# Kernel tuning notes

Hardware: AMD Instinct MI355X
Metric: run time of the kernel (lower is better)

The kernel has to match this reference:

```python
import jax, jax.numpy as jnp
import numpy as np

B, C, OUT, H, W, M1, M2, HID = 4, 64, 64, 256, 256, 32, 32, 64
COORD = C + 1  # MLP input: channels + 1 coordinate


def _lin(key, fan_in, fan_out):
    lim = 1.0 / np.sqrt(fan_in)
    kw, kb = jax.random.split(key)
    Wm = jax.random.uniform(kw, (fan_in, fan_out), minval=-lim, maxval=lim, dtype=jnp.float32)
    b = jax.random.uniform(kb, (fan_out,), minval=-lim, maxval=lim, dtype=jnp.float32)
    return Wm, b


def setup_inputs() -> dict:
    key = jax.random.key(0)
    ks = jax.random.split(key, 12)
    x = jax.random.normal(ks[0], (B, C, H, W), dtype=jnp.float32)
    # basis_w MLP: (C+1) -> HID -> HID -> 2*M2
    wW0, wb0 = _lin(ks[1], COORD, HID)
    wW1, wb1 = _lin(ks[2], HID, HID)
    wW2, wb2 = _lin(ks[3], HID, 2 * M2)
    # basis_h MLP: (C+1) -> HID -> HID -> 2*M1
    hW0, hb0 = _lin(ks[4], COORD, HID)
    hW1, hb1 = _lin(ks[5], HID, HID)
    hW2, hb2 = _lin(ks[6], HID, 2 * M1)
    std = (1.0 / (C + OUT)) ** 0.5
    Wf_re = std * jax.random.normal(ks[7], (C, OUT, M1, M2), dtype=jnp.float32)
    Wf_im = std * jax.random.normal(ks[8], (C, OUT, M1, M2), dtype=jnp.float32)
    mixer_w, mixer_b = _lin(ks[9], OUT, OUT)
    mixer_w = mixer_w.T  # (out, in) conv1x1 layout
    sc_w, sc_b = _lin(ks[10], C, OUT)
    sc_w = sc_w.T
    return {
        "x": x,
        "wW0": wW0, "wb0": wb0, "wW1": wW1, "wb1": wb1, "wW2": wW2, "wb2": wb2,
        "hW0": hW0, "hb0": hb0, "hW1": hW1, "hb1": hb1, "hW2": hW2, "hb2": hb2,
        "Wf_re": Wf_re, "Wf_im": Wf_im,
        "mixer_w": mixer_w, "mixer_b": mixer_b,
        "sc_w": sc_w, "sc_b": sc_b,
    }


def _gelu(v):
    return jax.nn.gelu(v, approximate=False)  # torch GELU is exact erf


def _cmlp(x, W0, b0, W1, b1, W2, b2, m):
    h = _gelu(x @ W0 + b0)
    h = _gelu(h @ W1 + b1)
    o = h @ W2 + b2
    return jax.lax.complex(o[..., :m], o[..., m:])


def reference(x, wW0, wb0, wW1, wb1, wW2, wb2,
              hW0, hb0, hW1, hb1, hW2, hb2,
              Wf_re, Wf_im, mixer_w, mixer_b, sc_w, sc_b):
    Bb, Cc, Hh, Ww = x.shape
    # --- W-direction basis: input is (values, w-coord) per pixel ---
    wc = jnp.linspace(-1.0, 1.0, Ww, dtype=jnp.float32)
    w_in = jnp.concatenate(
        [jnp.transpose(x, (0, 2, 3, 1)),
         jnp.broadcast_to(wc[None, None, :, None], (Bb, Hh, Ww, 1))], axis=-1)
    wb = _cmlp(w_in, wW0, wb0, wW1, wb1, wW2, wb2, M2)  # (B,H,W,m2) complex
    xc = x.astype(jnp.complex64)
    # separable transform along W: contract W against runtime basis
    tfw = jnp.einsum('bchw,bhwm->bchm', xc, wb)  # (B,C,H,m2)
    # --- H-direction basis: input is real part of W-transform + h-coord ---
    hcv = jnp.linspace(-1.0, 1.0, Hh, dtype=jnp.float32)
    h_in = jnp.concatenate(
        [jnp.transpose(tfw.real, (0, 3, 2, 1)),
         jnp.broadcast_to(hcv[None, None, :, None], (Bb, M2, Hh, 1))], axis=-1)
    hb = _cmlp(h_in, hW0, hb0, hW1, hb1, hW2, hb2, M1)  # (B,m2,H,m1) complex
    tfhw = jnp.einsum('bchm,bmhk->bckm', tfw, hb)  # (B,C,m1,m2)
    Wf = jax.lax.complex(Wf_re, Wf_im)  # (C_in, C_out, m1, m2)
    proc = jnp.einsum('bixy,oixy->boxy', tfhw, Wf)  # (B,out,m1,m2)
    # inverse transforms with conjugate-transposed bases
    rec = jnp.einsum('bokm,bmhk->bohm', proc, jnp.conj(hb))  # (B,out,H,m2)
    spatial = jnp.einsum('bohm,bhwm->bohw', rec, jnp.conj(wb)).real / (Hh * Ww)
    y = jnp.einsum('bchw,oc->bohw', spatial, mixer_w) + mixer_b[None, :, None, None]
    y = _gelu(y)
    y = y + jnp.einsum('bchw,oc->bohw', x, sc_w) + sc_b[None, :, None, None]
    return _gelu(y)
```

## Files before the change

kernel.cpp:

```cpp
#include <hip/hip_runtime.h>
#include <math.h>


typedef __attribute__((ext_vector_type(8))) short bf16x8;
typedef __attribute__((ext_vector_type(4))) float f32x4;

__device__ __forceinline__ float gelu_f(float v) {
    const float u = v * 0.70710678118654752440f;
    const float xa = fabsf(u);
    const float t = __builtin_amdgcn_rcpf(fmaf(0.3275911f, xa, 1.0f));
    float p = fmaf(1.061405429f, t, -1.453152027f);
    p = fmaf(p, t, 1.421413741f);
    p = fmaf(p, t, -0.284496736f);
    p = fmaf(p, t, 0.254829592f);
    p *= t;
    const float e = __expf(-xa * xa);
    float erfv = fmaf(-p, e, 1.0f);
    erfv = (u < 0.0f) ? -erfv : erfv;
    return 0.5f * v * (1.0f + erfv);
}

__device__ __forceinline__ unsigned short f2b(float f) {
    union { float f; unsigned int u; } v; v.f = f;
    unsigned int u = v.u + 0x7FFFu + ((v.u >> 16) & 1u);
    return (unsigned short)(u >> 16);
}
__device__ __forceinline__ float b2f(unsigned short b) {
    union { unsigned int u; float f; } v; v.u = ((unsigned int)b) << 16;
    return v.f;
}

__device__ __forceinline__ ushort4 butterfly_xT(const float4 v, int q) {
    const float bx = __shfl_xor(v.x, 1);
    const float by = __shfl_xor(v.y, 1);
    const float bz = __shfl_xor(v.z, 1);
    const float bw = __shfl_xor(v.w, 1);
    float4 s1;
    s1.x = ((q & 1) == 0) ? v.x : by;
    s1.y = ((q & 1) == 0) ? bx  : v.y;
    s1.z = ((q & 1) == 0) ? v.z : bw;
    s1.w = ((q & 1) == 0) ? bz  : v.w;
    const float cx = __shfl_xor(s1.x, 2);
    const float cy = __shfl_xor(s1.y, 2);
    const float cz = __shfl_xor(s1.z, 2);
    const float cw = __shfl_xor(s1.w, 2);
    float4 s2;
    s2.x = ((q & 2) == 0) ? s1.x : cz;
    s2.y = ((q & 2) == 0) ? s1.y : cw;
    s2.z = ((q & 2) == 0) ? cx   : s1.z;
    s2.w = ((q & 2) == 0) ? cy   : s1.w;
    ushort4 u;
    u.x = f2b(s2.x); u.y = f2b(s2.y); u.z = f2b(s2.z); u.w = f2b(s2.w);
    return u;
}

__global__ void k_prep(const float* __restrict__ wW0, const float* __restrict__ wW1,
                       const float* __restrict__ wW2,
                       const float* __restrict__ hW0, const float* __restrict__ hW1,
                       const float* __restrict__ hW2,
                       unsigned short* __restrict__ wT0, unsigned short* __restrict__ wT1,
                       unsigned short* __restrict__ wT2,
                       unsigned short* __restrict__ hT0, unsigned short* __restrict__ hT1,
                       unsigned short* __restrict__ hT2)
{
    const int t = threadIdx.x;
    for (int idx = t; idx < 64 * 96; idx += 256) {
        const int o = idx / 96, k = idx % 96;
        wT0[idx] = (k < 65) ? f2b(wW0[k * 64 + o]) : (unsigned short)0;
        hT0[idx] = (k < 65) ? f2b(hW0[k * 64 + o]) : (unsigned short)0;
    }
    for (int idx = t; idx < 4096; idx += 256) {
        const int o = idx >> 6, k = idx & 63;
        wT1[idx] = f2b(wW1[k * 64 + o]);
        wT2[idx] = f2b(wW2[k * 64 + o]);
        hT1[idx] = f2b(hW1[k * 64 + o]);
        hT2[idx] = f2b(hW2[k * 64 + o]);
    }
}

__global__ __launch_bounds__(256) void k_psum(const float* __restrict__ src,
                                              float* __restrict__ dst,
                                              int nparts, int part_stride)
{
    const int i = (blockIdx.x * 256 + threadIdx.x) * 4;
    float4 acc = *(const float4*)&src[i];
    for (int p = 1; p < nparts; ++p) {
        const float4 v = *(const float4*)&src[(size_t)p * part_stride + i];
        acc.x += v.x; acc.y += v.y; acc.z += v.z; acc.w += v.w;
    }
    *(float4*)&dst[i] = acc;
}

__global__ __launch_bounds__(256) void k_psum_procT(const float* __restrict__ src,
                                                    float* __restrict__ dst)
{
    const int idx = blockIdx.x * 256 + threadIdx.x;
    const int o = idx & 63, k = (idx >> 6) & 31, m = (idx >> 11) & 31, b = idx >> 16;
    const size_t in = (size_t)(b * 64 + o) * 1024 + k * 32 + m;
    const float re = src[in] + src[524288 + in];
    const float im = src[262144 + in] + src[524288 + 262144 + in];
    dst[idx] = re;
    dst[262144 + idx] = im;
}

template<bool GELU, int NKC>
__device__ __forceinline__ void mfma_layer_r(
    const bf16x8* __restrict__ wf,
    const unsigned short* __restrict__ sAct,
    unsigned short* __restrict__ dst,
    const float4 bv, int arow, int g, int wv)
{
    const int crow = 16 * wv + g * 4;
    const int sx7 = arow & 7, sx3 = arow & 3;
    const f32x4 zero = {0.f, 0.f, 0.f, 0.f};
    f32x4 acc[4] = {zero, zero, zero, zero};
#pragma unroll
    for (int kc = 0; kc < NKC; ++kc) {
        const int chraw = kc * 4 + g;
        const int ch = (chraw < 8) ? (chraw ^ sx7) : (8 + ((chraw - 8) ^ sx3));
#pragma unroll
        for (int nt = 0; nt < 4; ++nt) {
            const bf16x8 b = *(const bf16x8*)&sAct[(nt * 16 + arow) * 96 + ch * 8];
            acc[nt] = __builtin_amdgcn_mfma_f32_16x16x32_bf16(wf[kc], b, acc[nt], 0, 0, 0);
        }
    }
    const int chw = (crow >> 3) ^ sx7;
#pragma unroll
    for (int nt = 0; nt < 4; ++nt) {
        const int px = nt * 16 + arow;
        float v0 = acc[nt][0] + bv.x;
        float v1 = acc[nt][1] + bv.y;
        float v2 = acc[nt][2] + bv.z;
        float v3 = acc[nt][3] + bv.w;
        if (GELU) { v0 = gelu_f(v0); v1 = gelu_f(v1); v2 = gelu_f(v2); v3 = gelu_f(v3); }
        ushort4 u;
        u.x = f2b(v0); u.y = f2b(v1); u.z = f2b(v2); u.w = f2b(v3);
        *(ushort4*)&dst[px * 96 + chw * 8 + (crow & 7)] = u;
    }
}

__global__ __launch_bounds__(256) void k_wbtfw(
    const float* __restrict__ x,
    const unsigned short* __restrict__ wT0, const float* __restrict__ b0,
    const unsigned short* __restrict__ wT1, const float* __restrict__ b1,
    const unsigned short* __restrict__ wT2, const float* __restrict__ b2,
    unsigned short* __restrict__ wb_bf, unsigned short* __restrict__ xT_bf,
    float* __restrict__ tfwM)
{
    __shared__ __align__(16) unsigned short smem[20480];
    unsigned short* sA   = smem;
    unsigned short* sB   = smem + 6144;
    unsigned short* sXt  = smem + 12288;
    unsigned short* sWBt = smem + 16384;

    const int bh = blockIdx.x;
    const int b = bh >> 8, h = bh & 255;
    const int t = threadIdx.x;
    const int lane = t & 63, wv = t >> 6;
    const int arow = lane & 15, g = lane >> 4;
    const int crow = 16 * wv + g * 4;
    const int sx7 = arow & 7;
    const f32x4 zero = {0.f, 0.f, 0.f, 0.f};

    const int wrow = 16 * wv + arow;
    bf16x8 w0f[3], w1f[2], w2f[2];
#pragma unroll
    for (int kc = 0; kc < 3; ++kc)
        w0f[kc] = *(const bf16x8*)&wT0[wrow * 96 + (kc * 4 + g) * 8];
#pragma unroll
    for (int kc = 0; kc < 2; ++kc) {
        w1f[kc] = *(const bf16x8*)&wT1[wrow * 64 + (kc * 4 + g) * 8];
        w2f[kc] = *(const bf16x8*)&wT2[wrow * 64 + (kc * 4 + g) * 8];
    }
    const float4 bv0 = *(const float4*)&b0[crow];
    const float4 bv1 = *(const float4*)&b1[crow];
    const float4 bv2 = *(const float4*)&b2[crow];

    f32x4 atf[4] = {zero, zero, zero, zero};

    for (int wq = 0; wq < 4; ++wq) {
        const int w0 = wq * 64;
        __syncthreads();
        {
            const int q = lane & 3, wg = lane >> 2;
#pragma unroll
            for (int r = 0; r < 4; ++r) {
                const int cb = 16 * r + 4 * wv;
                const int c = cb + q;
                const float4 v = *(const float4*)&x[((size_t)(b * 64 + c) * 256 + h) * 256 + w0 + wg * 4];
                ushort4 ux;
                ux.x = f2b(v.x); ux.y = f2b(v.y); ux.z = f2b(v.z); ux.w = f2b(v.w);
                const int chx = (wg >> 1) ^ (c & 7);
                *(ushort4*)&sXt[c * 64 + chx * 8 + 4 * (wg & 1)] = ux;
                const ushort4 u = butterfly_xT(v, q);
                const int row = wg * 4 + q;
                const int cha = (cb >> 3) ^ (row & 7);
                *(ushort4*)&sA[row * 96 + cha * 8 + (cb & 7)] = u;
            }
        }
        if (t < 64) {
            const uint4 z = {0, 0, 0, 0};
#pragma unroll
            for (int j = 0; j < 4; ++j)
                *(uint4*)&sA[t * 96 + (8 + (j ^ (t & 3))) * 8] = z;
            sA[t * 96 + (8 + (t & 3)) * 8] = f2b((float)(w0 + t) * (2.0f / 255.0f) - 1.0f);
        }
        __syncthreads();
        const size_t pixbase = (size_t)(b * 256 + h) * 256 + w0;
#pragma unroll
        for (int r = 0; r < 2; ++r) {
            const int idx = r * 256 + t;
            const int px = idx >> 3, f = idx & 7;
            *(uint4*)&xT_bf[(pixbase + px) * 64 + f * 8] =
                *(const uint4*)&sA[px * 96 + ((f ^ (px & 7)) << 3)];
        }
        mfma_layer_r<true, 3>(w0f, sA, sB, bv0, arow, g, wv);
        __syncthreads();
        mfma_layer_r<true, 2>(w1f, sB, sA, bv1, arow, g, wv);
        __syncthreads();
        {
            f32x4 acc[4] = {zero, zero, zero, zero};
#pragma unroll
            for (int kc = 0; kc < 2; ++kc) {
                const int ch = (kc * 4 + g) ^ sx7;
#pragma unroll
                for (int nt = 0; nt < 4; ++nt) {
                    const bf16x8 bb = *(const bf16x8*)&sA[(nt * 16 + arow) * 96 + ch * 8];
                    acc[nt] = __builtin_amdgcn_mfma_f32_16x16x32_bf16(w2f[kc], bb, acc[nt], 0, 0, 0);
                }
            }
            const int chw = (crow >> 3) ^ sx7;
#pragma unroll
            for (int nt = 0; nt < 4; ++nt) {
                const int px = nt * 16 + arow;
                ushort4 u;
                u.x = f2b(acc[nt][0] + bv2.x);
                u.y = f2b(acc[nt][1] + bv2.y);
                u.z = f2b(acc[nt][2] + bv2.z);
                u.w = f2b(acc[nt][3] + bv2.w);
                *(ushort4*)&sB[px * 96 + chw * 8 + (crow & 7)] = u;
                const int ph = px >> 3, pl = px & 7;
                sWBt[(crow + 0) * 64 + ((ph ^ ((crow + 0) & 7)) << 3) + pl] = u.x;
                sWBt[(crow + 1) * 64 + ((ph ^ ((crow + 1) & 7)) << 3) + pl] = u.y;
                sWBt[(crow + 2) * 64 + ((ph ^ ((crow + 2) & 7)) << 3) + pl] = u.z;
                sWBt[(crow + 3) * 64 + ((ph ^ ((crow + 3) & 7)) << 3) + pl] = u.w;
            }
        }
        __syncthreads();
#pragma unroll
        for (int r = 0; r < 2; ++r) {
            const int idx = r * 256 + t;
            const int px = idx >> 3, f = idx & 7;
            *(uint4*)&wb_bf[(pixbase + px) * 64 + f * 8] =
                *(const uint4*)&sB[px * 96 + ((f ^ (px & 7)) << 3)];
        }
#pragma unroll
        for (int kc = 0; kc < 2; ++kc) {
            const int ch = (kc * 4 + g) ^ sx7;
            const bf16x8 a = *(const bf16x8*)&sWBt[(16 * wv + arow) * 64 + ch * 8];
#pragma unroll
            for (int nt = 0; nt < 4; ++nt) {
                const bf16x8 bb = *(const bf16x8*)&sXt[(nt * 16 + arow) * 64 + ch * 8];
                atf[nt] = __builtin_amdgcn_mfma_f32_16x16x32_bf16(a, bb, atf[nt], 0, 0, 0);
            }
        }
    }

    __syncthreads();
    float* sF = (float*)smem;
#pragma unroll
    for (int nt = 0; nt < 4; ++nt) {
        const int c = nt * 16 + arow;
#pragma unroll
        for (int j = 0; j < 4; ++j)
            sF[(crow + j) * 68 + c] = atf[nt][j];
    }
    __syncthreads();
#pragma unroll
    for (int r = 0; r < 4; ++r) {
        const int idx = r * 256 + t;
        const int m = idx >> 5, gg = idx & 31;
        float4 v;
        v.x = sF[m * 68 + gg * 2];
        v.y = sF[(m + 32) * 68 + gg * 2];
        v.z = sF[m * 68 + gg * 2 + 1];
        v.w = sF[(m + 32) * 68 + gg * 2 + 1];
        *(float4*)&tfwM[((size_t)(b * 32 + m) * 256 + h) * 128 + gg * 4] = v;
    }
}

__global__ __launch_bounds__(256) void k_hb_mlp3(
    const float* __restrict__ tfwM,
    const unsigned short* __restrict__ hT0, const float* __restrict__ b0,
    const unsigned short* __restrict__ hT1, const float* __restrict__ b1,
    const unsigned short* __restrict__ hT2, const float* __restrict__ b2,
    unsigned short* __restrict__ hb_bf)
{
    __shared__ __align__(16) unsigned short sA[64 * 96];
    __shared__ __align__(16) unsigned short sB[64 * 96];
    const int blk = blockIdx.x;
    const int bm = blk >> 2, hq = blk & 3;
    const int h0 = hq * 64;
    const int t = threadIdx.x;
    const int lane = t & 63, wv = t >> 6;
    const int arow = lane & 15, g = lane >> 4;
    const int crow = 16 * wv + g * 4;

    const int wrow = 16 * wv + arow;
    bf16x8 h0f[3], h1f[2], h2f[2];
#pragma unroll
    for (int kc = 0; kc < 3; ++kc)
        h0f[kc] = *(const bf16x8*)&hT0[wrow * 96 + (kc * 4 + g) * 8];
#pragma unroll
    for (int kc = 0; kc < 2; ++kc) {
        h1f[kc] = *(const bf16x8*)&hT1[wrow * 64 + (kc * 4 + g) * 8];
        h2f[kc] = *(const bf16x8*)&hT2[wrow * 64 + (kc * 4 + g) * 8];
    }
    const float4 bv0 = *(const float4*)&b0[crow];
    const float4 bv1 = *(const float4*)&b1[crow];
    const float4 bv2 = *(const float4*)&b2[crow];

#pragma unroll
    for (int r = 0; r < 4; ++r) {
        const int idx = r * 256 + t;
        const int p = idx >> 4, f = idx & 15;
        const float* src = &tfwM[(size_t)(bm * 256 + h0 + p) * 128 + f * 8];
        const float4 u0 = *(const float4*)&src[0];
        const float4 u1 = *(const float4*)&src[4];
        ushort4 u;
        u.x = f2b(u0.x); u.y = f2b(u0.z); u.z = f2b(u1.x); u.w = f2b(u1.z);
        const int ch = (f >> 1) ^ (p & 7);
        *(ushort4*)&sA[p * 96 + ch * 8 + 4 * (f & 1)] = u;
    }
    if (t < 64) {
        const uint4 z = {0, 0, 0, 0};
#pragma unroll
        for (int j = 0; j < 4; ++j)
            *(uint4*)&sA[t * 96 + (8 + (j ^ (t & 3))) * 8] = z;
        sA[t * 96 + (8 + (t & 3)) * 8] = f2b((float)(h0 + t) * (2.0f / 255.0f) - 1.0f);
    }
    __syncthreads();
    mfma_layer_r<true, 3>(h0f, sA, sB, bv0, arow, g, wv);
    __syncthreads();
    mfma_layer_r<true, 2>(h1f, sB, sA, bv1, arow, g, wv);
    __syncthreads();
    mfma_layer_r<false, 2>(h2f, sA, sB, bv2, arow, g, wv);
    __syncthreads();

    const size_t pixbase = (size_t)bm * 256 + h0;
#pragma unroll
    for (int r = 0; r < 2; ++r) {
        const int idx = r * 256 + t;
        const int px = idx >> 3, f = idx & 7;
        *(uint4*)&hb_bf[(pixbase + px) * 64 + f * 8] =
            *(const uint4*)&sB[px * 96 + ((f ^ (px & 7)) << 3)];
    }
}

__global__ __launch_bounds__(256) void k_tfhw3(
    const float* __restrict__ tfwM,
    const unsigned short* __restrict__ hb_bf,
    float* __restrict__ tfhw_p)
{
    __shared__ float hr[64 * 32];
    __shared__ float hi2[64 * 32];
    __shared__ float slab[32 * 64];
    const int blk = blockIdx.x;
    const int bm = blk >> 3, chalf = (blk >> 2) & 1, hq = blk & 3;
    const int b = bm >> 5, m = bm & 31;
    const int t = threadIdx.x;
#pragma unroll
    for (int r = 0; r < 2; ++r) {
        const int q = r * 256 + t;
        const int hl = q >> 3, f = q & 7;
        const uint4 raw = *(const uint4*)&hb_bf[((size_t)bm * 256 + hq * 64 + hl) * 64 + f * 8];
        const unsigned short* us = (const unsigned short*)&raw;
        float v[8];
#pragma unroll
        for (int j = 0; j < 8; ++j) v[j] = b2f(us[j]);
        float* dst = (f < 4) ? &hr[hl * 32 + f * 8] : &hi2[hl * 32 + (f - 4) * 8];
        float4 lo; lo.x = v[0]; lo.y = v[1]; lo.z = v[2]; lo.w = v[3];
        float4 hi; hi.x = v[4]; hi.y = v[5]; hi.z = v[6]; hi.w = v[7];
        *(float4*)&dst[0] = lo;
        *(float4*)&dst[4] = hi;
    }
    const int k = t & 31, cq = t >> 5;
    float accr[4] = {0.f, 0.f, 0.f, 0.f}, acci[4] = {0.f, 0.f, 0.f, 0.f};
    const size_t tbase = (size_t)bm * 32768;
    for (int ht = 0; ht < 2; ++ht) {
        __syncthreads();
#pragma unroll
        for (int r = 0; r < 2; ++r) {
            const int q = r * 256 + t;
            const int hl = q >> 3, f = q & 7;
            *(float4*)&slab[hl * 64 + f * 4] =
                *(const float4*)&tfwM[tbase + (size_t)(hq * 64 + ht * 32 + hl) * 128 + chalf * 64 + f * 4];
        }
        __syncthreads();
#pragma unroll 8
        for (int hl = 0; hl < 32; ++hl) {
            const float hrv = hr[(ht * 32 + hl) * 32 + k];
            const float hiv = hi2[(ht * 32 + hl) * 32 + k];
            const float4 u0 = *(const float4*)&slab[hl * 64 + cq * 8];
            const float4 u1 = *(const float4*)&slab[hl * 64 + cq * 8 + 4];
            accr[0] = fmaf(u0.x, hrv, fmaf(-u0.y, hiv, accr[0]));
            acci[0] = fmaf(u0.x, hiv, fmaf( u0.y, hrv, acci[0]));
            accr[1] = fmaf(u0.z, hrv, fmaf(-u0.w, hiv, accr[1]));
            acci[1] = fmaf(u0.z, hiv, fmaf( u0.w, hrv, acci[1]));
            accr[2] = fmaf(u1.x, hrv, fmaf(-u1.y, hiv, accr[2]));
            acci[2] = fmaf(u1.x, hiv, fmaf( u1.y, hrv, acci[2]));
            accr[3] = fmaf(u1.z, hrv, fmaf(-u1.w, hiv, accr[3]));
            acci[3] = fmaf(u1.z, hiv, fmaf( u1.w, hrv, acci[3]));
        }
    }
    float* tp = tfhw_p + (size_t)hq * 524288;
#pragma unroll
    for (int i = 0; i < 4; ++i) {
        const int c = chalf * 32 + cq * 4 + i;
        const size_t po = ((size_t)(b * 64 + c) * 32 + k) * 32 + m;
        tp[po] = accr[i];
        tp[262144 + po] = acci[i];
    }
}

__global__ __launch_bounds__(256) void k_proc2(
    const float* __restrict__ tfhw,
    const float* __restrict__ Wf_re, const float* __restrict__ Wf_im,
    float* __restrict__ proc_p)
{
    const int blk = blockIdx.x;
    const int o = blk >> 3, kq = (blk >> 1) & 3, chalf = blk & 1;
    const int t = threadIdx.x;
    const int mo = kq * 256 + t;
    const float* tre = tfhw;
    const float* tim = tfhw + 262144;
    float accr[4] = {0.f, 0.f, 0.f, 0.f}, acci[4] = {0.f, 0.f, 0.f, 0.f};
    for (int cc = 0; cc < 32; ++cc) {
        const int c = chalf * 32 + cc;
        const float wfr = Wf_re[(size_t)(c * 64 + o) * 1024 + mo];
        const float wfi = Wf_im[(size_t)(c * 64 + o) * 1024 + mo];
#pragma unroll
        for (int bb = 0; bb < 4; ++bb) {
            const float tr = tre[(size_t)(bb * 64 + c) * 1024 + mo];
            const float ti = tim[(size_t)(bb * 64 + c) * 1024 + mo];
            accr[bb] = fmaf(tr, wfr, fmaf(-ti, wfi, accr[bb]));
            acci[bb] = fmaf(tr, wfi, fmaf(ti, wfr, acci[bb]));
        }
    }
    float* pp = proc_p + (size_t)chalf * 524288;
#pragma unroll
    for (int bb = 0; bb < 4; ++bb) {
        pp[(size_t)(bb * 64 + o) * 1024 + mo] = accr[bb];
        pp[262144 + (size_t)(bb * 64 + o) * 1024 + mo] = acci[bb];
    }
}

__global__ __launch_bounds__(256) void k_rec4(
    const float* __restrict__ procT,
    const unsigned short* __restrict__ hb_bf,
    unsigned short* __restrict__ recO)
{
    __shared__ float lhr[32 * 32];
    __shared__ float lhi[32 * 32];
    const int blk = blockIdx.x;
    const int bm = blk >> 3, hq = blk & 7;
    const int b = bm >> 5, m = bm & 31;
    const int t = threadIdx.x;
    {
        const int hl = t >> 3, f = t & 7;
        const uint4 raw = *(const uint4*)&hb_bf[((size_t)bm * 256 + hq * 32 + hl) * 64 + f * 8];
        const unsigned short* us = (const unsigned short*)&raw;
        float v[8];
#pragma unroll
        for (int j = 0; j < 8; ++j) v[j] = b2f(us[j]);
        float* dst = (f < 4) ? &lhr[hl * 32 + f * 8] : &lhi[hl * 32 + (f - 4) * 8];
        float4 lo; lo.x = v[0]; lo.y = v[1]; lo.z = v[2]; lo.w = v[3];
        float4 hi; hi.x = v[4]; hi.y = v[5]; hi.z = v[6]; hi.w = v[7];
        *(float4*)&dst[0] = lo;
        *(float4*)&dst[4] = hi;
    }
    const int o = t & 63, hg = t >> 6;
    const float* pr = procT + (size_t)(b * 32 + m) * 2048 + o;
    const float* pi = pr + 262144;
    float Pr[32], Pi[32];
#pragma unroll
    for (int k = 0; k < 32; ++k) {
        Pr[k] = pr[k * 64];
        Pi[k] = pi[k * 64];
    }
    __syncthreads();
    for (int hh = 0; hh < 8; ++hh) {
        const int hl = hg * 8 + hh;
        float ar = 0.f, ai = 0.f;
#pragma unroll
        for (int k4 = 0; k4 < 8; ++k4) {
            const float4 hr4 = *(const float4*)&lhr[hl * 32 + k4 * 4];
            const float4 hi4 = *(const float4*)&lhi[hl * 32 + k4 * 4];
            ar = fmaf(Pr[k4*4+0], hr4.x, fmaf(Pi[k4*4+0], hi4.x, ar));
            ai = fmaf(Pi[k4*4+0], hr4.x, fmaf(-Pr[k4*4+0], hi4.x, ai));
            ar = fmaf(Pr[k4*4+1], hr4.y, fmaf(Pi[k4*4+1], hi4.y, ar));
            ai = fmaf(Pi[k4*4+1], hr4.y, fmaf(-Pr[k4*4+1], hi4.y, ai));
            ar = fmaf(Pr[k4*4+2], hr4.z, fmaf(Pi[k4*4+2], hi4.z, ar));
            ai = fmaf(Pi[k4*4+2], hr4.z, fmaf(-Pr[k4*4+2], hi4.z, ai));
            ar = fmaf(Pr[k4*4+3], hr4.w, fmaf(Pi[k4*4+3], hi4.w, ar));
            ai = fmaf(Pi[k4*4+3], hr4.w, fmaf(-Pr[k4*4+3], hi4.w, ai));
        }
        const int h = hq * 32 + hl;
        const size_t rb = ((size_t)(b * 256 + h) * 64 + o) * 64;
        recO[rb + m]      = f2b(ar);
        recO[rb + 32 + m] = f2b(ai);
    }
}

__global__ __launch_bounds__(256) void k_final4(
    const unsigned short* __restrict__ xT_bf,
    const unsigned short* __restrict__ wb_bf,
    const unsigned short* __restrict__ recO,
    const float* __restrict__ mw, const float* __restrict__ mb,
    const float* __restrict__ scw, const float* __restrict__ scb,
    float* __restrict__ out)
{
    constexpr int LD = 72;
    __shared__ __align__(16) unsigned short sWb[64 * LD];
    __shared__ __align__(16) unsigned short sR [64 * LD];
    __shared__ __align__(16) unsigned short sX [64 * LD];
    __shared__ __align__(16) unsigned short sS [64 * LD];
    const int blk = blockIdx.x;
    const int b = blk >> 10, h = (blk >> 2) & 255, wq = blk & 3;
    const int w0 = wq * 64;
    const int t = threadIdx.x;
    const int lane = t & 63, wv = t >> 6;
    const size_t pixbase = (size_t)(b * 256 + h) * 256 + w0;

#pragma unroll
    for (int r = 0; r < 2; ++r) {
        const int idx = r * 256 + t;
        const int px = idx >> 3, f = idx & 7;
        *(uint4*)&sWb[px * LD + f * 8] = *(const uint4*)&wb_bf[(pixbase + px) * 64 + f * 8];
    }
    const size_t recbase = (size_t)(b * 256 + h) * 4096;
#pragma unroll
    for (int r = 0; r < 2; ++r) {
        const int idx = r * 256 + t;
        const int o = idx >> 3, f = idx & 7;
        *(uint4*)&sR[o * LD + f * 8] = *(const uint4*)&recO[recbase + (size_t)o * 64 + f * 8];
    }
#pragma unroll
    for (int r = 0; r < 2; ++r) {
        const int idx = r * 256 + t;
        const int px = idx >> 3, f = idx & 7;
        *(uint4*)&sX[px * LD + f * 8] = *(const uint4*)&xT_bf[(pixbase + px) * 64 + f * 8];
    }
    __syncthreads();

    const int arow = lane & 15;
    const int koff = (lane >> 4) * 8;
    const f32x4 zero = {0.f, 0.f, 0.f, 0.f};

    f32x4 accA[4] = {zero, zero, zero, zero};
#pragma unroll
    for (int kc = 0; kc < 2; ++kc) {
        const bf16x8 a = *(const bf16x8*)&sR[(16 * wv + arow) * LD + kc * 32 + koff];
#pragma unroll
        for (int nt = 0; nt < 4; ++nt) {
            const bf16x8 bb = *(const bf16x8*)&sWb[(nt * 16 + arow) * LD + kc * 32 + koff];
            accA[nt] = __builtin_amdgcn_mfma_f32_16x16x32_bf16(a, bb, accA[nt], 0, 0, 0);
        }
    }
    __syncthreads();

    const int crow = 16 * wv + (lane >> 4) * 4;
#pragma unroll
    for (int nt = 0; nt < 4; ++nt) {
        const int px = nt * 16 + arow;
#pragma unroll
        for (int j = 0; j < 4; ++j)
            sS[px * LD + crow + j] = f2b(accA[nt][j] * (1.0f / 65536.0f));
    }
#pragma unroll
    for (int r = 0; r < 4; ++r) {
        const int idx = r * 256 + t;
        const int o = idx >> 4, cq = idx & 15;
        const float4 v1 = *(const float4*)&mw[o * 64 + cq * 4];
        ushort4 u1;
        u1.x = f2b(v1.x); u1.y = f2b(v1.y); u1.z = f2b(v1.z); u1.w = f2b(v1.w);
        *(ushort4*)&sWb[o * LD + cq * 4] = u1;
        const float4 v2 = *(const float4*)&scw[o * 64 + cq * 4];
        ushort4 u2;
        u2.x = f2b(v2.x); u2.y = f2b(v2.y); u2.z = f2b(v2.z); u2.w = f2b(v2.w);
        *(ushort4*)&sR[o * LD + cq * 4] = u2;
    }
    __syncthreads();

    f32x4 accB[4] = {zero, zero, zero, zero};
    f32x4 accC[4] = {zero, zero, zero, zero};
#pragma unroll
    for (int kc = 0; kc < 2; ++kc) {
        const bf16x8 am = *(const bf16x8*)&sWb[(16 * wv + arow) * LD + kc * 32 + koff];
        const bf16x8 as = *(const bf16x8*)&sR [(16 * wv + arow) * LD + kc * 32 + koff];
#pragma unroll
        for (int nt = 0; nt < 4; ++nt) {
            const bf16x8 bs = *(const bf16x8*)&sS[(nt * 16 + arow) * LD + kc * 32 + koff];
            const bf16x8 bx = *(const bf16x8*)&sX[(nt * 16 + arow) * LD + kc * 32 + koff];
            accB[nt] = __builtin_amdgcn_mfma_f32_16x16x32_bf16(am, bs, accB[nt], 0, 0, 0);
            accC[nt] = __builtin_amdgcn_mfma_f32_16x16x32_bf16(as, bx, accC[nt], 0, 0, 0);
        }
    }

#pragma unroll
    for (int nt = 0; nt < 4; ++nt) {
        const int px = nt * 16 + arow;
#pragma unroll
        for (int j = 0; j < 4; ++j) {
            const int o = crow + j;
            const float y = gelu_f(accB[nt][j] + mb[o]);
            const float z = y + accC[nt][j] + scb[o];
            out[((size_t)(b * 64 + o) * 256 + h) * 256 + w0 + px] = gelu_f(z);
        }
    }
}

extern "C" void kernel_launch(void* const* d_in, const int* in_sizes, int n_in,
                              void* d_out, int out_size, void* d_ws, size_t ws_size,
                              hipStream_t stream) {
    const float* x    = (const float*)d_in[0];
    const float* wW0  = (const float*)d_in[1];
    const float* wb0  = (const float*)d_in[2];
    const float* wW1  = (const float*)d_in[3];
    const float* wb1  = (const float*)d_in[4];
    const float* wW2  = (const float*)d_in[5];
    const float* wb2  = (const float*)d_in[6];
    const float* hW0  = (const float*)d_in[7];
    const float* hb0  = (const float*)d_in[8];
    const float* hW1  = (const float*)d_in[9];
    const float* hb1  = (const float*)d_in[10];
    const float* hW2  = (const float*)d_in[11];
    const float* hb2  = (const float*)d_in[12];
    const float* Wf_re = (const float*)d_in[13];
    const float* Wf_im = (const float*)d_in[14];
    const float* mw   = (const float*)d_in[15];
    const float* mbv  = (const float*)d_in[16];
    const float* scw  = (const float*)d_in[17];
    const float* scb  = (const float*)d_in[18];

    char* base = (char*)d_ws;
    unsigned short* wb_bf = (unsigned short*)(base + 0);
    unsigned short* xT_bf = (unsigned short*)(base + 33554432);
    float* tfwM   = (float*)(base + 67108864);
    unsigned short* hb_bf = (unsigned short*)(base + 83886080);
    float* tfhw_p = (float*)(base + 88080384);
    float* tfhw   = (float*)(base + 96468992);
    float* proc_p = (float*)(base + 98566144);
    float* procT  = (float*)(base + 102760448);
    unsigned short* recO = (unsigned short*)(base + 104857600);
    unsigned short* wT0 = (unsigned short*)(base + 113246208);
    unsigned short* wT1 = (unsigned short*)(base + 113258496);
    unsigned short* wT2 = (unsigned short*)(base + 113266688);
    unsigned short* hT0 = (unsigned short*)(base + 113274880);
    unsigned short* hT1 = (unsigned short*)(base + 113287168);
    unsigned short* hT2 = (unsigned short*)(base + 113295360);

    k_prep<<<1, 256, 0, stream>>>(wW0, wW1, wW2, hW0, hW1, hW2,
                                  wT0, wT1, wT2, hT0, hT1, hT2);
    k_wbtfw<<<1024, 256, 0, stream>>>(x, wT0, wb0, wT1, wb1, wT2, wb2,
                                      wb_bf, xT_bf, tfwM);
    k_hb_mlp3<<<512, 256, 0, stream>>>(tfwM, hT0, hb0, hT1, hb1, hT2, hb2, hb_bf);
    k_tfhw3<<<1024, 256, 0, stream>>>(tfwM, hb_bf, tfhw_p);
    k_psum<<<1024, 256, 0, stream>>>(tfhw_p, tfhw, 4, 524288);
    k_proc2<<<512, 256, 0, stream>>>(tfhw, Wf_re, Wf_im, proc_p);
    k_psum_procT<<<1024, 256, 0, stream>>>(proc_p, procT);
    k_rec4<<<1024, 256, 0, stream>>>(procT, hb_bf, recO);
    k_final4<<<4096, 256, 0, stream>>>(xT_bf, wb_bf, recO, mw, mbv, scw, scb,
                                       (float*)d_out);
}
```

Baseline: 193.2 us.

## Drop xT intermediate, store tfwM as bf16, prefetch x tiles in W-basis kernel

Removes the bf16 transposed-x workspace buffer (32 MB write plus read). k_final4 now re-reads fp32 x and transposes it in registers with the butterfly shuffle. The tfwM intermediate is stored as bf16 instead of fp32, which halves its write and read traffic in the two H-direction kernels. k_wbtfw also software-prefetches the next x tile into registers during compute. In exchange, k_tfhw3 now reads a bf16-rounded tfwM, which may reduce accuracy, and k_final4 reads twice as many bytes of x as it did of xT.

```diff
diff --git a/kernel.cpp b/kernel.cpp
--- a/kernel.cpp
+++ b/kernel.cpp
@@ -54,6 +54,20 @@
     return u;
 }
 
+__device__ __forceinline__ void stage_xT(const float* __restrict__ x,
+    unsigned short* __restrict__ sA, int b, int h, int w0, int t, int LD)
+{
+    const int lane = t & 63, wv = t >> 6;
+    const int q = lane & 3, wg = lane >> 2;
+#pragma unroll
+    for (int r = 0; r < 4; ++r) {
+        const int cb = (r * 4 + wv) * 4;
+        const float4 v = *(const float4*)&x[((size_t)(b * 64 + cb + q) * 256 + h) * 256 + w0 + wg * 4];
+        const ushort4 u = butterfly_xT(v, q);
+        *(ushort4*)&sA[(wg * 4 + q) * LD + cb] = u;
+    }
+}
+
 __global__ void k_prep(const float* __restrict__ wW0, const float* __restrict__ wW1,
                        const float* __restrict__ wW2,
                        const float* __restrict__ hW0, const float* __restrict__ hW1,
@@ -139,13 +153,20 @@
     }
 }
 
+__device__ __forceinline__ float4 load_xtile(const float* __restrict__ x,
+    int b, int h, int w0, int lane, int wv, int r)
+{
+    const int q = lane & 3, wg = lane >> 2;
+    const int cb = 16 * r + 4 * wv;
+    return *(const float4*)&x[((size_t)(b * 64 + cb + q) * 256 + h) * 256 + w0 + wg * 4];
+}
+
 __global__ __launch_bounds__(256) void k_wbtfw(
     const float* __restrict__ x,
     const unsigned short* __restrict__ wT0, const float* __restrict__ b0,
     const unsigned short* __restrict__ wT1, const float* __restrict__ b1,
     const unsigned short* __restrict__ wT2, const float* __restrict__ b2,
-    unsigned short* __restrict__ wb_bf, unsigned short* __restrict__ xT_bf,
-    float* __restrict__ tfwM)
+    unsigned short* __restrict__ wb_bf, unsigned short* __restrict__ tfwM)
 {
     __shared__ __align__(16) unsigned short smem[20480];
     unsigned short* sA   = smem;
@@ -178,6 +199,10 @@
 
     f32x4 atf[4] = {zero, zero, zero, zero};
 
+    float4 xv[4];
+#pragma unroll
+    for (int r = 0; r < 4; ++r) xv[r] = load_xtile(x, b, h, 0, lane, wv, r);
+
     for (int wq = 0; wq < 4; ++wq) {
         const int w0 = wq * 64;
         __syncthreads();
@@ -187,7 +212,7 @@
             for (int r = 0; r < 4; ++r) {
                 const int cb = 16 * r + 4 * wv;
                 const int c = cb + q;
-                const float4 v = *(const float4*)&x[((size_t)(b * 64 + c) * 256 + h) * 256 + w0 + wg * 4];
+                const float4 v = xv[r];
                 ushort4 ux;
                 ux.x = f2b(v.x); ux.y = f2b(v.y); ux.z = f2b(v.z); ux.w = f2b(v.w);
                 const int chx = (wg >> 1) ^ (c & 7);
@@ -205,15 +230,11 @@
                 *(uint4*)&sA[t * 96 + (8 + (j ^ (t & 3))) * 8] = z;
             sA[t * 96 + (8 + (t & 3)) * 8] = f2b((float)(w0 + t) * (2.0f / 255.0f) - 1.0f);
         }
+        const int w0n = ((wq + 1) & 3) * 64;
+        float4 xn[4];
+#pragma unroll
+        for (int r = 0; r < 4; ++r) xn[r] = load_xtile(x, b, h, w0n, lane, wv, r);
         __syncthreads();
-        const size_t pixbase = (size_t)(b * 256 + h) * 256 + w0;
-#pragma unroll
-        for (int r = 0; r < 2; ++r) {
-            const int idx = r * 256 + t;
-            const int px = idx >> 3, f = idx & 7;
-            *(uint4*)&xT_bf[(pixbase + px) * 64 + f * 8] =
-                *(const uint4*)&sA[px * 96 + ((f ^ (px & 7)) << 3)];
-        }
         mfma_layer_r<true, 3>(w0f, sA, sB, bv0, arow, g, wv);
         __syncthreads();
         mfma_layer_r<true, 2>(w1f, sB, sA, bv1, arow, g, wv);
@@ -247,6 +268,7 @@
             }
         }
         __syncthreads();
+        const size_t pixbase = (size_t)(b * 256 + h) * 256 + w0;
 #pragma unroll
         for (int r = 0; r < 2; ++r) {
             const int idx = r * 256 + t;
@@ -264,6 +286,8 @@
                 atf[nt] = __builtin_amdgcn_mfma_f32_16x16x32_bf16(a, bb, atf[nt], 0, 0, 0);
             }
         }
+#pragma unroll
+        for (int r = 0; r < 4; ++r) xv[r] = xn[r];
     }
 
     __syncthreads();
@@ -280,17 +304,17 @@
     for (int r = 0; r < 4; ++r) {
         const int idx = r * 256 + t;
         const int m = idx >> 5, gg = idx & 31;
-        float4 v;
-        v.x = sF[m * 68 + gg * 2];
-        v.y = sF[(m + 32) * 68 + gg * 2];
-        v.z = sF[m * 68 + gg * 2 + 1];
-        v.w = sF[(m + 32) * 68 + gg * 2 + 1];
-        *(float4*)&tfwM[((size_t)(b * 32 + m) * 256 + h) * 128 + gg * 4] = v;
+        ushort4 u;
+        u.x = f2b(sF[m * 68 + gg * 2]);
+        u.y = f2b(sF[(m + 32) * 68 + gg * 2]);
+        u.z = f2b(sF[m * 68 + gg * 2 + 1]);
+        u.w = f2b(sF[(m + 32) * 68 + gg * 2 + 1]);
+        *(ushort4*)&tfwM[((size_t)(b * 32 + m) * 256 + h) * 128 + gg * 4] = u;
     }
 }
 
 __global__ __launch_bounds__(256) void k_hb_mlp3(
-    const float* __restrict__ tfwM,
+    const unsigned short* __restrict__ tfwM,
     const unsigned short* __restrict__ hT0, const float* __restrict__ b0,
     const unsigned short* __restrict__ hT1, const float* __restrict__ b1,
     const unsigned short* __restrict__ hT2, const float* __restrict__ b2,
@@ -324,11 +348,10 @@
     for (int r = 0; r < 4; ++r) {
         const int idx = r * 256 + t;
         const int p = idx >> 4, f = idx & 15;
-        const float* src = &tfwM[(size_t)(bm * 256 + h0 + p) * 128 + f * 8];
-        const float4 u0 = *(const float4*)&src[0];
-        const float4 u1 = *(const float4*)&src[4];
+        const uint4 raw = *(const uint4*)&tfwM[((size_t)(bm * 256 + h0 + p)) * 128 + f * 8];
+        const unsigned short* s = (const unsigned short*)&raw;
         ushort4 u;
-        u.x = f2b(u0.x); u.y = f2b(u0.z); u.z = f2b(u1.x); u.w = f2b(u1.z);
+        u.x = s[0]; u.y = s[2]; u.z = s[4]; u.w = s[6];
         const int ch = (f >> 1) ^ (p & 7);
         *(ushort4*)&sA[p * 96 + ch * 8 + 4 * (f & 1)] = u;
     }
@@ -358,7 +381,7 @@
 }
 
 __global__ __launch_bounds__(256) void k_tfhw3(
-    const float* __restrict__ tfwM,
+    const unsigned short* __restrict__ tfwM,
     const unsigned short* __restrict__ hb_bf,
     float* __restrict__ tfhw_p)
 {
@@ -389,12 +412,15 @@
     const size_t tbase = (size_t)bm * 32768;
     for (int ht = 0; ht < 2; ++ht) {
         __syncthreads();
-#pragma unroll
-        for (int r = 0; r < 2; ++r) {
-            const int q = r * 256 + t;
-            const int hl = q >> 3, f = q & 7;
-            *(float4*)&slab[hl * 64 + f * 4] =
-                *(const float4*)&tfwM[tbase + (size_t)(hq * 64 + ht * 32 + hl) * 128 + chalf * 64 + f * 4];
+        {
+            const int hl = t >> 3, f = t & 7;
+            const uint4 raw = *(const uint4*)&tfwM[tbase + (size_t)(hq * 64 + ht * 32 + hl) * 128 + chalf * 64 + f * 8];
+            const unsigned short* s = (const unsigned short*)&raw;
+            float4 lo, hi;
+            lo.x = b2f(s[0]); lo.y = b2f(s[1]); lo.z = b2f(s[2]); lo.w = b2f(s[3]);
+            hi.x = b2f(s[4]); hi.y = b2f(s[5]); hi.z = b2f(s[6]); hi.w = b2f(s[7]);
+            *(float4*)&slab[hl * 64 + f * 8] = lo;
+            *(float4*)&slab[hl * 64 + f * 8 + 4] = hi;
         }
         __syncthreads();
 #pragma unroll 8
@@ -513,7 +539,7 @@
 }
 
 __global__ __launch_bounds__(256) void k_final4(
-    const unsigned short* __restrict__ xT_bf,
+    const float* __restrict__ x,
     const unsigned short* __restrict__ wb_bf,
     const unsigned short* __restrict__ recO,
     const float* __restrict__ mw, const float* __restrict__ mb,
@@ -545,12 +571,7 @@
         const int o = idx >> 3, f = idx & 7;
         *(uint4*)&sR[o * LD + f * 8] = *(const uint4*)&recO[recbase + (size_t)o * 64 + f * 8];
     }
-#pragma unroll
-    for (int r = 0; r < 2; ++r) {
-        const int idx = r * 256 + t;
-        const int px = idx >> 3, f = idx & 7;
-        *(uint4*)&sX[px * LD + f * 8] = *(const uint4*)&xT_bf[(pixbase + px) * 64 + f * 8];
-    }
+    stage_xT(x, sX, b, h, w0, t, LD);
     __syncthreads();
 
     const int arow = lane & 15;
@@ -645,31 +666,30 @@
 
     char* base = (char*)d_ws;
     unsigned short* wb_bf = (unsigned short*)(base + 0);
-    unsigned short* xT_bf = (unsigned short*)(base + 33554432);
-    float* tfwM   = (float*)(base + 67108864);
-    unsigned short* hb_bf = (unsigned short*)(base + 83886080);
-    float* tfhw_p = (float*)(base + 88080384);
-    float* tfhw   = (float*)(base + 96468992);
-    float* proc_p = (float*)(base + 98566144);
-    float* procT  = (float*)(base + 102760448);
-    unsigned short* recO = (unsigned short*)(base + 104857600);
-    unsigned short* wT0 = (unsigned short*)(base + 113246208);
-    unsigned short* wT1 = (unsigned short*)(base + 113258496);
-    unsigned short* wT2 = (unsigned short*)(base + 113266688);
-    unsigned short* hT0 = (unsigned short*)(base + 113274880);
-    unsigned short* hT1 = (unsigned short*)(base + 113287168);
-    unsigned short* hT2 = (unsigned short*)(base + 113295360);
+    unsigned short* tfwM  = (unsigned short*)(base + 33554432);
+    unsigned short* hb_bf = (unsigned short*)(base + 41943040);
+    float* tfhw_p = (float*)(base + 46137344);
+    float* tfhw   = (float*)(base + 54525952);
+    float* proc_p = (float*)(base + 56623104);
+    float* procT  = (float*)(base + 60817408);
+    unsigned short* recO = (unsigned short*)(base + 62914560);
+    unsigned short* wT0 = (unsigned short*)(base + 71303168);
+    unsigned short* wT1 = (unsigned short*)(base + 71315456);
+    unsigned short* wT2 = (unsigned short*)(base + 71323648);
+    unsigned short* hT0 = (unsigned short*)(base + 71331840);
+    unsigned short* hT1 = (unsigned short*)(base + 71344128);
+    unsigned short* hT2 = (unsigned short*)(base + 71352320);
 
     k_prep<<<1, 256, 0, stream>>>(wW0, wW1, wW2, hW0, hW1, hW2,
                                   wT0, wT1, wT2, hT0, hT1, hT2);
     k_wbtfw<<<1024, 256, 0, stream>>>(x, wT0, wb0, wT1, wb1, wT2, wb2,
-                                      wb_bf, xT_bf, tfwM);
+                                      wb_bf, tfwM);
     k_hb_mlp3<<<512, 256, 0, stream>>>(tfwM, hT0, hb0, hT1, hb1, hT2, hb2, hb_bf);
     k_tfhw3<<<1024, 256, 0, stream>>>(tfwM, hb_bf, tfhw_p);
     k_psum<<<1024, 256, 0, stream>>>(tfhw_p, tfhw, 4, 524288);
     k_proc2<<<512, 256, 0, stream>>>(tfhw, Wf_re, Wf_im, proc_p);
     k_psum_procT<<<1024, 256, 0, stream>>>(proc_p, procT);
     k_rec4<<<1024, 256, 0, stream>>>(procT, hb_bf, recO);
-    k_final4<<<4096, 256, 0, stream>>>(xT_bf, wb_bf, recO, mw, mbv, scw, scb,
+    k_final4<<<4096, 256, 0, stream>>>(x, wb_bf, recO, mw, mbv, scw, scb,
                                        (float*)d_out);
 }
```

Result: faster. 180.1 us (-6.8%).
